# Optimization experiments

Hardware: AMD Instinct MI355X
Metric: run time of the kernel (lower is better)

Reference implementation:

```python
import jax, jax.numpy as jnp
import numpy as np

HID = 1024

def setup_inputs() -> dict:
    key = jax.random.key(0)
    k1, k2, k3, k4, k5 = jax.random.split(key, 5)
    B, S, H = 16, 2048, HID
    queries = jax.random.normal(k1, (B, H), dtype=jnp.float32)
    keys = jax.random.normal(k2, (B, S, H), dtype=jnp.float32)
    values = jax.random.normal(k3, (B, S, H), dtype=jnp.float32)
    # additive_attention params: Linear(2H->H), ReLU, Linear(H->1)
    s1 = 1.0 / np.sqrt(2 * H)
    s2 = 1.0 / np.sqrt(H)
    W1 = jax.random.uniform(k4, (2 * H, H), dtype=jnp.float32, minval=-s1, maxval=s1)
    b1 = jnp.zeros((H,), dtype=jnp.float32)
    W2 = jax.random.uniform(k5, (H, 1), dtype=jnp.float32, minval=-s2, maxval=s2)
    b2 = jnp.zeros((1,), dtype=jnp.float32)
    return {"queries": queries, "keys": keys, "values": values,
            "W1": W1, "b1": b1, "W2": W2, "b2": b2}

def reference(queries, keys, values, W1, b1, W2, b2):
    B, S, H = keys.shape
    # concat expanded query with keys along feature dim: [B,S,2H]
    q_exp = jnp.broadcast_to(queries[:, None, :], (B, S, H))
    concat = jnp.concatenate([q_exp, keys], axis=-1)
    h = jax.nn.relu(jnp.einsum('bsf,fh->bsh', concat, W1) + b1)
    scores = jnp.einsum('bsh,ho->bso', h, W2) + b2          # [B,S,1]
    alphas = jax.nn.softmax(scores, axis=1)                  # softmax over seq
    # context = alphas^T @ values : [B,1,H]
    context = jnp.einsum('bso,bsh->boh', alphas, values)
    return (context, alphas)
```

## Files before the change

kernel.cpp:

```cpp
#include <hip/hip_runtime.h>

#define HID 1024
#define SEQ 2048
#define NB  16

typedef __attribute__((ext_vector_type(8))) short bf16x8;
typedef __attribute__((ext_vector_type(4))) float f32x4;

static __device__ __forceinline__ short f2bf(float f) {
    union { float f; unsigned u; } v; v.f = f;
    unsigned u = v.u + 0x7fffu + ((v.u >> 16) & 1u);
    return (short)(u >> 16);
}
static __device__ __forceinline__ unsigned pk2h(float a, float b) {
    unsigned r;
    asm("v_cvt_pk_bf16_f32 %0, %1, %2" : "=v"(r) : "v"(a), "v"(b));
    return r;
}
static __device__ __forceinline__ void glds16(const void* g, void* l) {
    __builtin_amdgcn_global_load_lds(
        (const __attribute__((address_space(1))) unsigned*)g,
        (__attribute__((address_space(3))) unsigned*)l, 16, 0, 0);
}

__global__ __launch_bounds__(256) void prep_all(const float* __restrict__ W1,
                                                const float* __restrict__ queries,
                                                const float* __restrict__ b1,
                                                const float* __restrict__ keys,
                                                short* __restrict__ w1t,
                                                float* __restrict__ qproj_part,
                                                short* __restrict__ kbf,
                                                int nconv) {
    __shared__ float shmem[2048];
    const int tid = threadIdx.x;
    int bw = blockIdx.x;

    if (bw < 32) {
        const int fc = bw >> 2, nc = bw & 3;
        const int f0 = fc * 128, n0 = nc * 256;
#pragma unroll
        for (int j = 0; j < 8; ++j) {
            const int idx = tid * 8 + j;
            const int b = idx >> 7, f = idx & 127;
            shmem[idx] = queries[b * HID + f0 + f];
        }
        __syncthreads();
        float acc[16];
        const float bv = (fc == 0) ? b1[n0 + tid] : 0.0f;
#pragma unroll
        for (int b = 0; b < 16; ++b) acc[b] = bv;
        for (int f = 0; f < 128; ++f) {
            const float w = W1[(size_t)(f0 + f) * HID + n0 + tid];
#pragma unroll
            for (int b = 0; b < 16; ++b)
                acc[b] += shmem[b * 128 + f] * w;
        }
#pragma unroll
        for (int b = 0; b < 16; ++b)
            qproj_part[(size_t)(fc * 16 + b) * HID + n0 + tid] = acc[b];
        return;
    }
    bw -= 32;
    if (bw < 1024) {
        float (*t)[33] = (float(*)[33])shmem;
        const int k0 = (bw & 31) * 32;
        const int n0 = (bw >> 5) * 32;
        const int tx = tid & 31, ty = tid >> 5;
#pragma unroll
        for (int i = 0; i < 32; i += 8)
            t[ty + i][tx] = W1[(size_t)(HID + k0 + ty + i) * HID + n0 + tx];
        __syncthreads();
#pragma unroll
        for (int i = 0; i < 32; i += 8)
            w1t[(size_t)(n0 + ty + i) * HID + k0 + tx] = f2bf(t[tx][ty + i]);
        return;
    }
    bw -= 1024;
    if (bw < nconv) {
        const size_t i = ((size_t)bw * 256 + tid) * 8;
        const float4 a = *(const float4*)(keys + i);
        const float4 b = *(const float4*)(keys + i + 4);
        int4 o;
        o.x = (int)pk2h(a.x, a.y); o.y = (int)pk2h(a.z, a.w);
        o.z = (int)pk2h(b.x, b.y); o.w = (int)pk2h(b.z, b.w);
        *(int4*)(kbf + i) = o;
    }
}

template<int PRE>
__global__ __launch_bounds__(256, 4) void score_gemm(const float* __restrict__ keys,
                                                     const short* __restrict__ kbf,
                                                     const short* __restrict__ w1t,
                                                     const float* __restrict__ qproj_part,
                                                     const float* __restrict__ W2,
                                                     float* __restrict__ scores_part) {
    __shared__ short As[128 * 32];
    __shared__ short Bs[128 * 32];
    __shared__ float red[4][64];

    const int tid  = threadIdx.x;
    const int lane = tid & 63;
    const int wave = tid >> 6;
    const int id   = blockIdx.x;
    const int n_blk = (id >> 3) & 7;
    const int m_blk = (id >> 6) * 8 + (id & 7);
    const int n0 = n_blk * 128;
    const int m0 = m_blk * 128;
    const int batch = m0 >> 11;
    const int wm = wave >> 1, wn = wave & 1;
    const int q = lane >> 4, c = lane & 15;
    const int xr = (c >> 1) & 3;

    const int lrow = lane >> 2;
    const int lk   = ((lane & 3) ^ ((lane >> 3) & 3)) << 3;
    const short* bsrc = w1t + (size_t)(n0 + lrow) * HID + lk;
    const short* asrc = kbf + (size_t)(m0 + lrow) * HID + lk;

    const int ar  = tid >> 1;
    const int ah  = (tid & 1) * 16;
    const int g_ar = (ar >> 1) & 3;
    const int as0 = (((ah >> 3) + 0) ^ g_ar) << 3;
    const int as1 = (((ah >> 3) + 1) ^ g_ar) << 3;
    const float* afsrc = keys + (size_t)(m0 + ar) * HID + ah;

    f32x4 acc[4][4] = {};

    for (int k0 = 0; k0 < HID; k0 += 32) {
#pragma unroll
        for (int call = 0; call < 2; ++call) {
            const int rbase = (wave * 2 + call) * 16;
            glds16(bsrc + (size_t)rbase * HID + k0, &Bs[rbase * 32]);
        }
        if (PRE) {
#pragma unroll
            for (int call = 0; call < 2; ++call) {
                const int rbase = (wave * 2 + call) * 16;
                glds16(asrc + (size_t)rbase * HID + k0, &As[rbase * 32]);
            }
        } else {
            const float4 v0 = *(const float4*)(afsrc + k0 + 0);
            const float4 v1 = *(const float4*)(afsrc + k0 + 4);
            const float4 v2 = *(const float4*)(afsrc + k0 + 8);
            const float4 v3 = *(const float4*)(afsrc + k0 + 12);
            int4 o0, o1;
            o0.x = (int)pk2h(v0.x, v0.y); o0.y = (int)pk2h(v0.z, v0.w);
            o0.z = (int)pk2h(v1.x, v1.y); o0.w = (int)pk2h(v1.z, v1.w);
            o1.x = (int)pk2h(v2.x, v2.y); o1.y = (int)pk2h(v2.z, v2.w);
            o1.z = (int)pk2h(v3.x, v3.y); o1.w = (int)pk2h(v3.z, v3.w);
            *(int4*)&As[ar * 32 + as0] = o0;
            *(int4*)&As[ar * 32 + as1] = o1;
        }
        __syncthreads();

        bf16x8 af[4], bf[4];
#pragma unroll
        for (int i = 0; i < 4; ++i)
            af[i] = *(const bf16x8*)&As[(wm * 64 + i * 16 + c) * 32 + ((q ^ xr) << 3)];
#pragma unroll
        for (int i = 0; i < 4; ++i)
            bf[i] = *(const bf16x8*)&Bs[(wn * 64 + i * 16 + c) * 32 + ((q ^ xr) << 3)];
#pragma unroll
        for (int mi = 0; mi < 4; ++mi)
#pragma unroll
            for (int ni = 0; ni < 4; ++ni)
                acc[mi][ni] = __builtin_amdgcn_mfma_f32_16x16x32_bf16(af[mi], bf[ni], acc[mi][ni], 0, 0, 0);
        __syncthreads();
    }

    const float* w2 = W2 + n0 + wn * 64;
    float psum[4][4] = {};
#pragma unroll
    for (int ni = 0; ni < 4; ++ni) {
        const int n = n0 + wn * 64 + ni * 16 + c;
        float qv = 0.f;
#pragma unroll
        for (int p = 0; p < 8; ++p)
            qv += qproj_part[(size_t)(p * 16 + batch) * HID + n];
        const float wv = w2[ni * 16 + c];
#pragma unroll
        for (int mi = 0; mi < 4; ++mi)
#pragma unroll
            for (int r = 0; r < 4; ++r)
                psum[mi][r] += fmaxf(acc[mi][ni][r] + qv, 0.f) * wv;
    }
#pragma unroll
    for (int m = 1; m < 16; m <<= 1)
#pragma unroll
        for (int mi = 0; mi < 4; ++mi)
#pragma unroll
            for (int r = 0; r < 4; ++r)
                psum[mi][r] += __shfl_xor(psum[mi][r], m, 64);
    if (c == 0) {
#pragma unroll
        for (int mi = 0; mi < 4; ++mi)
#pragma unroll
            for (int r = 0; r < 4; ++r)
                red[wave][mi * 16 + q * 4 + r] = psum[mi][r];
    }
    __syncthreads();
    if (tid < 128) {
        const int wm2 = tid >> 6, idx = tid & 63;
        scores_part[(size_t)n_blk * (SEQ * NB) + m0 + wm2 * 64 + idx] =
            red[wm2 * 2][idx] + red[wm2 * 2 + 1][idx];
    }
}

__global__ __launch_bounds__(256) void softmax_k(const float* __restrict__ scores_part,
                                                 float* __restrict__ alphas) {
    __shared__ float red[256];
    const int b = blockIdx.x;
    const int tid = threadIdx.x;
    const float* sp = scores_part + b * SEQ;

    float loc[8];
    float mx = -1e30f;
#pragma unroll
    for (int i = 0; i < 8; ++i) {
        const int s = tid + i * 256;
        float v = 0.f;
#pragma unroll
        for (int p = 0; p < 8; ++p)
            v += sp[(size_t)p * (SEQ * NB) + s];
        loc[i] = v;
        mx = fmaxf(mx, v);
    }
    red[tid] = mx; __syncthreads();
    for (int s = 128; s > 0; s >>= 1) {
        if (tid < s) red[tid] = fmaxf(red[tid], red[tid + s]);
        __syncthreads();
    }
    mx = red[0]; __syncthreads();
    float sum = 0.f;
#pragma unroll
    for (int i = 0; i < 8; ++i) { loc[i] = expf(loc[i] - mx); sum += loc[i]; }
    red[tid] = sum; __syncthreads();
    for (int s = 128; s > 0; s >>= 1) {
        if (tid < s) red[tid] += red[tid + s];
        __syncthreads();
    }
    const float inv = 1.0f / red[0];
#pragma unroll
    for (int i = 0; i < 8; ++i) alphas[b * SEQ + tid + i * 256] = loc[i] * inv;
}

__global__ __launch_bounds__(256) void context_part_k(const float* __restrict__ alphas,
                                                      const float* __restrict__ values,
                                                      float* __restrict__ ctx_part) {
    __shared__ float al[64];
    const int b = blockIdx.y;
    const int sb = blockIdx.x;
    const int s0 = sb * 64;
    const int tid = threadIdx.x;
    if (tid < 64) al[tid] = alphas[b * SEQ + s0 + tid];
    __syncthreads();
    const int col = tid * 4;
    float4 acc = {0.f, 0.f, 0.f, 0.f};
#pragma unroll 8
    for (int i = 0; i < 64; ++i) {
        const float a = al[i];
        const float4 v = *(const float4*)(values + (size_t)(b * SEQ + s0 + i) * HID + col);
        acc.x += a * v.x; acc.y += a * v.y; acc.z += a * v.z; acc.w += a * v.w;
    }
    *(float4*)(ctx_part + (size_t)(sb * NB + b) * HID + col) = acc;
}

__global__ __launch_bounds__(256) void ctx_reduce_k(const float* __restrict__ ctx_part,
                                                    float* __restrict__ context) {
    const int b = blockIdx.x;
    const int col = threadIdx.x * 4;
    float4 s = {0.f, 0.f, 0.f, 0.f};
#pragma unroll
    for (int p = 0; p < 32; ++p) {
        const float4 v = *(const float4*)(ctx_part + (size_t)(p * NB + b) * HID + col);
        s.x += v.x; s.y += v.y; s.z += v.z; s.w += v.w;
    }
    *(float4*)(context + b * HID + col) = s;
}

extern "C" void kernel_launch(void* const* d_in, const int* in_sizes, int n_in,
                              void* d_out, int out_size, void* d_ws, size_t ws_size,
                              hipStream_t stream) {
    const float* queries = (const float*)d_in[0];
    const float* keys    = (const float*)d_in[1];
    const float* values  = (const float*)d_in[2];
    const float* W1      = (const float*)d_in[3];
    const float* b1      = (const float*)d_in[4];
    const float* W2      = (const float*)d_in[5];

    float* out_ctx   = (float*)d_out;
    float* out_alpha = (float*)d_out + NB * HID;

    char* ws = (char*)d_ws;
    float* scores_part = (float*)ws;
    float* qproj_part  = (float*)(ws + 1048576);
    float* ctx_part    = (float*)(ws + 1572864);
    short* w1t         = (short*)(ws + 3670016);
    short* kbf         = (short*)(ws + 5767168);

    const bool pre = ws_size >= 72876032ull;
    const int nconv = pre ? 16384 : 0;

    prep_all<<<32 + 1024 + nconv, 256, 0, stream>>>(
        W1, queries, b1, keys, w1t, qproj_part, kbf, nconv);

    if (pre)
        score_gemm<1><<<2048, 256, 0, stream>>>(keys, kbf, w1t, qproj_part, W2, scores_part);
    else
        score_gemm<0><<<2048, 256, 0, stream>>>(keys, kbf, w1t, qproj_part, W2, scores_part);

    softmax_k<<<NB, 256, 0, stream>>>(scores_part, out_alpha);
    context_part_k<<<dim3(32, NB), 256, 0, stream>>>(out_alpha, values, ctx_part);
    ctx_reduce_k<<<NB, 256, 0, stream>>>(ctx_part, out_ctx);
}
```

Before: 372.7 us.

## Fuse softmax, context partials and reduction into one tail kernel with atomics

Replaces the three-kernel tail (softmax, per-chunk context partials, partial reduction) with a single kernel. Each block recomputes the per-batch max and sum over the full sequence, then computes its own 64 alphas and accumulates its context slice into the output with atomicAdd. The output is zeroed by extra blocks in the prep kernel, and the ctx_part workspace is dropped. This removes two launches and the partial-buffer round trip, at the cost of 32x redundant softmax reductions per batch, atomic contention, and nondeterministic summation order.

```diff
diff --git a/kernel.cpp b/kernel.cpp
--- a/kernel.cpp
+++ b/kernel.cpp
@@ -30,6 +30,7 @@
                                                 short* __restrict__ w1t,
                                                 float* __restrict__ qproj_part,
                                                 short* __restrict__ kbf,
+                                                float* __restrict__ out_ctx,
                                                 int nconv) {
     __shared__ float shmem[2048];
     const int tid = threadIdx.x;
@@ -76,6 +77,12 @@
         return;
     }
     bw -= 1024;
+    if (bw < 16) {
+        float4 z = {0.f, 0.f, 0.f, 0.f};
+        *(float4*)(out_ctx + (size_t)(bw * 256 + tid) * 4) = z;
+        return;
+    }
+    bw -= 16;
     if (bw < nconv) {
         const size_t i = ((size_t)bw * 256 + tid) * 8;
         const float4 a = *(const float4*)(keys + i);
@@ -205,10 +212,15 @@
     }
 }
 
-__global__ __launch_bounds__(256) void softmax_k(const float* __restrict__ scores_part,
-                                                 float* __restrict__ alphas) {
+__global__ __launch_bounds__(256) void tail_k(const float* __restrict__ scores_part,
+                                              const float* __restrict__ values,
+                                              float* __restrict__ alphas,
+                                              float* __restrict__ out_ctx) {
     __shared__ float red[256];
-    const int b = blockIdx.x;
+    __shared__ float al[64];
+    const int b   = blockIdx.y;
+    const int sb  = blockIdx.x;
+    const int s0  = sb * 64;
     const int tid = threadIdx.x;
     const float* sp = scores_part + b * SEQ;
 
@@ -232,27 +244,25 @@
     mx = red[0]; __syncthreads();
     float sum = 0.f;
 #pragma unroll
-    for (int i = 0; i < 8; ++i) { loc[i] = expf(loc[i] - mx); sum += loc[i]; }
+    for (int i = 0; i < 8; ++i) sum += expf(loc[i] - mx);
     red[tid] = sum; __syncthreads();
     for (int s = 128; s > 0; s >>= 1) {
         if (tid < s) red[tid] += red[tid + s];
         __syncthreads();
     }
     const float inv = 1.0f / red[0];
-#pragma unroll
-    for (int i = 0; i < 8; ++i) alphas[b * SEQ + tid + i * 256] = loc[i] * inv;
-}
-
-__global__ __launch_bounds__(256) void context_part_k(const float* __restrict__ alphas,
-                                                      const float* __restrict__ values,
-                                                      float* __restrict__ ctx_part) {
-    __shared__ float al[64];
-    const int b = blockIdx.y;
-    const int sb = blockIdx.x;
-    const int s0 = sb * 64;
-    const int tid = threadIdx.x;
-    if (tid < 64) al[tid] = alphas[b * SEQ + s0 + tid];
+
+    if (tid < 64) {
+        float v = 0.f;
+#pragma unroll
+        for (int p = 0; p < 8; ++p)
+            v += sp[(size_t)p * (SEQ * NB) + s0 + tid];
+        const float a = expf(v - mx) * inv;
+        al[tid] = a;
+        alphas[b * SEQ + s0 + tid] = a;
+    }
     __syncthreads();
+
     const int col = tid * 4;
     float4 acc = {0.f, 0.f, 0.f, 0.f};
 #pragma unroll 8
@@ -261,20 +271,11 @@
         const float4 v = *(const float4*)(values + (size_t)(b * SEQ + s0 + i) * HID + col);
         acc.x += a * v.x; acc.y += a * v.y; acc.z += a * v.z; acc.w += a * v.w;
     }
-    *(float4*)(ctx_part + (size_t)(sb * NB + b) * HID + col) = acc;
-}
-
-__global__ __launch_bounds__(256) void ctx_reduce_k(const float* __restrict__ ctx_part,
-                                                    float* __restrict__ context) {
-    const int b = blockIdx.x;
-    const int col = threadIdx.x * 4;
-    float4 s = {0.f, 0.f, 0.f, 0.f};
-#pragma unroll
-    for (int p = 0; p < 32; ++p) {
-        const float4 v = *(const float4*)(ctx_part + (size_t)(p * NB + b) * HID + col);
-        s.x += v.x; s.y += v.y; s.z += v.z; s.w += v.w;
-    }
-    *(float4*)(context + b * HID + col) = s;
+    float* cp = out_ctx + b * HID + col;
+    atomicAdd(cp + 0, acc.x);
+    atomicAdd(cp + 1, acc.y);
+    atomicAdd(cp + 2, acc.z);
+    atomicAdd(cp + 3, acc.w);
 }
 
 extern "C" void kernel_launch(void* const* d_in, const int* in_sizes, int n_in,
@@ -293,22 +294,19 @@
     char* ws = (char*)d_ws;
     float* scores_part = (float*)ws;
     float* qproj_part  = (float*)(ws + 1048576);
-    float* ctx_part    = (float*)(ws + 1572864);
-    short* w1t         = (short*)(ws + 3670016);
-    short* kbf         = (short*)(ws + 5767168);
-
-    const bool pre = ws_size >= 72876032ull;
+    short* w1t         = (short*)(ws + 1572864);
+    short* kbf         = (short*)(ws + 3670016);
+
+    const bool pre = ws_size >= 70778880ull;
     const int nconv = pre ? 16384 : 0;
 
-    prep_all<<<32 + 1024 + nconv, 256, 0, stream>>>(
-        W1, queries, b1, keys, w1t, qproj_part, kbf, nconv);
+    prep_all<<<32 + 1024 + 16 + nconv, 256, 0, stream>>>(
+        W1, queries, b1, keys, w1t, qproj_part, kbf, out_ctx, nconv);
 
     if (pre)
         score_gemm<1><<<2048, 256, 0, stream>>>(keys, kbf, w1t, qproj_part, W2, scores_part);
     else
         score_gemm<0><<<2048, 256, 0, stream>>>(keys, kbf, w1t, qproj_part, W2, scores_part);
 
-    softmax_k<<<NB, 256, 0, stream>>>(scores_part, out_alpha);
-    context_part_k<<<dim3(32, NB), 256, 0, stream>>>(out_alpha, values, ctx_part);
-    ctx_reduce_k<<<NB, 256, 0, stream>>>(ctx_part, out_ctx);
-}
+    tail_k<<<dim3(32, NB), 256, 0, stream>>>(scores_part, values, out_alpha, out_ctx);
+}
```

Result: no change. 369.0 us (-1.0%).
